# Optimization experiments

Measured on AMD Instinct MI355X. Metric: run time of the kernel, lower is better.

Reference implementation:

```python
import jax, jax.numpy as jnp
import numpy as np

TEMP = 0.07
NUM_CLASSES = 4

def setup_inputs() -> dict:
    key = jax.random.key(0)
    k1, k2 = jax.random.split(key)
    features_in = jax.random.normal(k1, (4, 64, 2048), dtype=jnp.float32)
    labels_in = jax.random.randint(k2, (4, 2048), 0, NUM_CLASSES, dtype=jnp.int64)
    return {"features_in": features_in, "labels_in": labels_in}

def reference(features_in, labels_in):
    B, C, N = features_in.shape
    M = B * N
    # torch .view(C, B*N): row-major reinterpret of contiguous [B,C,N]
    feats = features_in.reshape(C, M).T            # [M, C]
    labels = labels_in.reshape(-1)                 # [M]

    # per-class keep probability: min(750/(count+1), 1), gathered by label
    counts = jnp.bincount(labels, length=NUM_CLASSES)
    keep_p = jnp.minimum(750.0 / (counts.astype(jnp.float32) + 1.0), 1.0)
    p = keep_p[labels]                             # [M]
    sel = jax.random.bernoulli(jax.random.key(42), p)  # [M] bool, stochastic subsample

    # L2 normalize rows; original divides by norms of already-normalized rows (==1)
    nv = feats / jnp.linalg.norm(feats, axis=1, keepdims=True)
    sim = nv @ nv.T                                # [M, M] cosine similarities
    dp = jnp.exp(sim / TEMP)
    dp = dp * (1.0 - jnp.eye(M, dtype=dp.dtype))   # zero the diagonal

    same = labels[:, None] == labels[None, :]
    pair = sel[:, None] & sel[None, :]             # both points kept
    pos = jnp.sum(jnp.where(same & pair, dp, 0.0), axis=1)
    neg = jnp.sum(jnp.where((~same) & pair, dp, 0.0), axis=1)

    frac = pos / (pos + neg)
    per = -jnp.log(jnp.where(sel, frac, 1.0))      # guard unselected rows
    n_sel = jnp.maximum(jnp.sum(sel), 1)
    loss = jnp.sum(jnp.where(sel, per, 0.0)) / n_sel
    return loss
```

## Files before the change

### kernel.cpp

```cpp
#include <hip/hip_runtime.h>
#include <hip/hip_bf16.h>

#define M_TOT 8192
#define NCLS 4
#define NSEL_CAP 4096
#define NT 64

typedef __attribute__((ext_vector_type(8)))  short short8v;
typedef __attribute__((ext_vector_type(16))) float f32x16;

__device__ __forceinline__ void async_copy16(const void* gsrc, void* ldst) {
#if defined(__HIP_DEVICE_COMPILE__)
    __builtin_amdgcn_global_load_lds(
        (const __attribute__((address_space(1))) void*)gsrc,
        (__attribute__((address_space(3))) void*)ldst, 16, 0, 0);
#endif
}

__device__ __forceinline__ unsigned int rotl32(unsigned int x, unsigned int r) {
    return (x << r) | (x >> (32u - r));
}

__device__ __forceinline__ uint2 threefry_pair_key42(unsigned int j) {
    const unsigned int ks0 = 0u;
    const unsigned int ks1 = 42u;
    const unsigned int ks2 = 0x1BD11BDAu ^ 0u ^ 42u;
    unsigned int x0 = j + ks0;
    unsigned int x1 = (j + 4096u) + ks1;
#define TF_RND(r) { x0 += x1; x1 = rotl32(x1, (r)); x1 ^= x0; }
    TF_RND(13u) TF_RND(15u) TF_RND(26u) TF_RND(6u)
    x0 += ks1; x1 += ks2 + 1u;
    TF_RND(17u) TF_RND(29u) TF_RND(16u) TF_RND(24u)
    x0 += ks2; x1 += ks0 + 2u;
    TF_RND(13u) TF_RND(15u) TF_RND(26u) TF_RND(6u)
    x0 += ks0; x1 += ks1 + 3u;
    TF_RND(17u) TF_RND(29u) TF_RND(16u) TF_RND(24u)
    x0 += ks1; x1 += ks2 + 4u;
    TF_RND(13u) TF_RND(15u) TF_RND(26u) TF_RND(6u)
    x0 += ks2; x1 += ks0 + 5u;
#undef TF_RND
    return make_uint2(x0, x1);
}

__device__ __forceinline__ float bits_to_unit(unsigned int bits) {
    return __uint_as_float((bits >> 9) | 0x3F800000u) - 1.0f;
}

__device__ __forceinline__ unsigned short f2bf(float x) {
    const unsigned int u = __float_as_uint(x);
    return (unsigned short)((u + 0x7FFFu + ((u >> 16) & 1u)) >> 16);
}
__device__ __forceinline__ float bf2f(unsigned short b) {
    return __uint_as_float(((unsigned int)b) << 16);
}

#define NV_OFS(plane, c, p) (((((plane) << 3) + (c)) << 12) + (p))

__global__ __launch_bounds__(256) void select_norm_kernel(
        const float* __restrict__ features,
        const int* __restrict__ labels,
        int* __restrict__ nsel_g,
        int* __restrict__ lab_sel,
        unsigned short* __restrict__ nv,
        float* __restrict__ pos,
        float* __restrict__ neg) {
    __shared__ int   hist[NCLS];
    __shared__ float keepp[NCLS];
    __shared__ int   wtot[4];
    __shared__ int   lds_m[NSEL_CAP];
    const int t = threadIdx.x, b = blockIdx.x;
    const int lane = t & 63, w = t >> 6;

    const int gid = b * 256 + t;
    if (gid < NSEL_CAP) { pos[gid] = 0.0f; neg[gid] = 0.0f; }
    if (t < NCLS) hist[t] = 0;
    __syncthreads();

    {
        const int m0 = t * 32;
        int c0 = 0, c1 = 0, c2 = 0, c3 = 0;
        for (int r = 0; r < 32; ++r) {
            const int lab = labels[m0 + r];
            c0 += (lab == 0); c1 += (lab == 1); c2 += (lab == 2); c3 += (lab == 3);
        }
        int cc[4] = {c0, c1, c2, c3};
        #pragma unroll
        for (int cls = 0; cls < NCLS; ++cls) {
            int v = cc[cls];
            for (int off = 32; off > 0; off >>= 1) v += __shfl_down(v, off, 64);
            if (lane == 0) atomicAdd(&hist[cls], v);
        }
    }
    __syncthreads();
    if (t < NCLS) keepp[t] = fminf(750.0f / ((float)hist[t] + 1.0f), 1.0f);
    __syncthreads();

    const int jb = t * 16;
    unsigned int flags = 0u;
    int cnt = 0;
    for (int r = 0; r < 16; ++r) {
        const uint2 bb = threefry_pair_key42((unsigned int)(jb + r));
        if (bits_to_unit(bb.x) < keepp[labels[jb + r]])        { flags |= 1u << r;        ++cnt; }
        if (bits_to_unit(bb.y) < keepp[labels[jb + r + 4096]]) { flags |= 1u << (16 + r); ++cnt; }
    }
    int x = cnt;
    #pragma unroll
    for (int off = 1; off < 64; off <<= 1) {
        const int y = __shfl_up(x, off, 64);
        if (lane >= off) x += y;
    }
    if (lane == 63) wtot[w] = x;
    const int excl = x - cnt;
    __syncthreads();
    int base = excl;
    for (int w2 = 0; w2 < w; ++w2) base += wtot[w2];
    const int nsel = wtot[0] + wtot[1] + wtot[2] + wtot[3];
    if (b == 0 && t == 0) *nsel_g = nsel;
    for (int r = 0; r < 16; ++r) {
        if (flags & (1u << r))        lds_m[base++] = jb + r;
        if (flags & (1u << (16 + r))) lds_m[base++] = jb + r + 4096;
    }
    __syncthreads();

    const int p  = b * 32 + (t >> 3);
    const int kg = t & 7;
    if (p >= nsel) return;
    const int m = lds_m[p];
    if (kg == 0) lab_sel[p] = labels[m];
    float v[8];
    float ss = 0.0f;
    #pragma unroll
    for (int q = 0; q < 8; ++q) {
        v[q] = features[(kg * 8 + q) * M_TOT + m];
        ss += v[q] * v[q];
    }
    ss += __shfl_xor(ss, 1, 8);
    ss += __shfl_xor(ss, 2, 8);
    ss += __shfl_xor(ss, 4, 8);
    const float rn = rsqrtf(ss);
    unsigned short hs[8], ls[8];
    #pragma unroll
    for (int q = 0; q < 8; ++q) {
        const float xx = v[q] * rn;
        const unsigned short h = f2bf(xx);
        hs[q] = h;
        ls[q] = f2bf(xx - bf2f(h));
    }
    *(uint4*)&nv[NV_OFS(0, kg, p) * 8] = *(const uint4*)hs;
    *(uint4*)&nv[NV_OFS(1, kg, p) * 8] = *(const uint4*)ls;
}

#define EXP2_SCALE 20.609929155556605f

__global__ __launch_bounds__(256, 4) void pair_kernel(
        const unsigned short* __restrict__ nv,
        const int* __restrict__ lab_sel,
        const int* __restrict__ nsel_g,
        float* __restrict__ pos,
        float* __restrict__ neg) {
    const int nsel = *nsel_g;
    const int it = blockIdx.y, jt = blockIdx.x;
    const int i0 = it * 64, j0 = jt * 64;
    if (i0 >= nsel || j0 >= nsel) return;

    __shared__ __align__(16) unsigned short frags[2][2][8][64][8];
    __shared__ int La[64], Lb[64];

    const int t = threadIdx.x;
    const int wave = t >> 6, lane = t & 63;

    #pragma unroll
    for (int it8 = 0; it8 < 8; ++it8) {
        const int combo = it8 * 4 + wave;
        const int side  = combo >> 4;
        const int plane = (combo >> 3) & 1;
        const int c     = combo & 7;
        const int base0 = (side ? j0 : i0);
        async_copy16(&nv[NV_OFS(plane, c, base0 + lane) * 8],
                     &frags[side][plane][c][lane][0]);
    }
    if (t < 64)       La[t]      = lab_sel[i0 + t];
    else if (t < 128) Lb[t - 64] = lab_sel[j0 + t - 64];
    __syncthreads();

    const int qi = (wave >> 1) * 32, qj = (wave & 1) * 32;
    const int half = lane >> 5, l31 = lane & 31;
    const int ra = qi + l31, rb = qj + l31;

    f32x16 acc;
    #pragma unroll
    for (int r = 0; r < 16; ++r) acc[r] = 0.0f;

    #pragma unroll
    for (int s = 0; s < 4; ++s) {
        const int c = 2 * s + half;
        const short8v ah = *(const short8v*)&frags[0][0][c][ra][0];
        const short8v al = *(const short8v*)&frags[0][1][c][ra][0];
        const short8v bh = *(const short8v*)&frags[1][0][c][rb][0];
        const short8v bl = *(const short8v*)&frags[1][1][c][rb][0];
        acc = __builtin_amdgcn_mfma_f32_32x32x16_bf16(ah, bh, acc, 0, 0, 0);
        acc = __builtin_amdgcn_mfma_f32_32x32x16_bf16(ah, bl, acc, 0, 0, 0);
        acc = __builtin_amdgcn_mfma_f32_32x32x16_bf16(al, bh, acc, 0, 0, 0);
    }

    const int colL = qj + l31;
    const int jg = j0 + colL;
    const int Lj = Lb[colL];
    float cp = 0.0f, cn = 0.0f;
    #pragma unroll
    for (int r = 0; r < 16; ++r) {
        const int rowL = qi + (r & 3) + 8 * (r >> 2) + 4 * half;
        const int ig = i0 + rowL;
        const bool valid = (ig < nsel) && (jg < nsel) && (ig != jg);
        const float d = valid ? exp2f(acc[r] * EXP2_SCALE) : 0.0f;
        if (La[rowL] == Lj) cp += d; else cn += d;
    }
    cp += __shfl_xor(cp, 32, 64);
    cn += __shfl_xor(cn, 32, 64);
    if (half == 0 && jg < nsel) {
        atomicAdd(&pos[jg], cp);
        atomicAdd(&neg[jg], cn);
    }
}

__global__ void loss_kernel(const float* __restrict__ pos,
                            const float* __restrict__ neg,
                            const int* __restrict__ nsel_g,
                            float* __restrict__ out) {
    const int nsel = *nsel_g;
    float s = 0.0f;
    for (int i = threadIdx.x; i < nsel; i += 256) {
        const float fr = pos[i] / (pos[i] + neg[i]);
        s += -logf(fr);
    }
    __shared__ float red[256];
    red[threadIdx.x] = s;
    __syncthreads();
    for (int off = 128; off > 0; off >>= 1) {
        if (threadIdx.x < off) red[threadIdx.x] += red[threadIdx.x + off];
        __syncthreads();
    }
    if (threadIdx.x == 0) out[0] = red[0] / (float)(nsel > 0 ? nsel : 1);
}

extern "C" void kernel_launch(void* const* d_in, const int* in_sizes, int n_in,
                              void* d_out, int out_size, void* d_ws, size_t ws_size,
                              hipStream_t stream) {
    const float* features = (const float*)d_in[0];
    const int*   labels   = (const int*)d_in[1];
    float*       out      = (float*)d_out;
    char*        ws       = (char*)d_ws;

    int*   nsel_g   = (int*)(ws);
    int*   lab_sel  = (int*)(ws + 1024);
    float* pos      = (float*)(ws + 1024 + 16384);
    float* neg      = pos + NSEL_CAP;
    unsigned short* nv = (unsigned short*)(ws + 1024 + 16384 + 32768);

    select_norm_kernel<<<128, 256, 0, stream>>>(features, labels, nsel_g, lab_sel,
                                                nv, pos, neg);
    pair_kernel<<<dim3(NT, NT), 256, 0, stream>>>(nv, lab_sel, nsel_g, pos, neg);
    loss_kernel<<<1, 256, 0, stream>>>(pos, neg, nsel_g, out);
}
```

Before: 82.71 us.

## Normalize features by source tile with coalesced loads instead of gathered selections

```diff
diff --git a/kernel.cpp b/kernel.cpp
--- a/kernel.cpp
+++ b/kernel.cpp
@@ -67,13 +67,15 @@
     __shared__ int   hist[NCLS];
     __shared__ float keepp[NCLS];
     __shared__ int   wtot[4];
-    __shared__ int   lds_m[NSEL_CAP];
+    __shared__ int   slot_local[64];
+    __shared__ float tile[64][65];
     const int t = threadIdx.x, b = blockIdx.x;
     const int lane = t & 63, w = t >> 6;
 
     const int gid = b * 256 + t;
     if (gid < NSEL_CAP) { pos[gid] = 0.0f; neg[gid] = 0.0f; }
     if (t < NCLS) hist[t] = 0;
+    if (t < 64) slot_local[t] = -1;
     __syncthreads();
 
     {
@@ -117,37 +119,61 @@
     const int nsel = wtot[0] + wtot[1] + wtot[2] + wtot[3];
     if (b == 0 && t == 0) *nsel_g = nsel;
     for (int r = 0; r < 16; ++r) {
-        if (flags & (1u << r))        lds_m[base++] = jb + r;
-        if (flags & (1u << (16 + r))) lds_m[base++] = jb + r + 4096;
-    }
-    __syncthreads();
-
-    const int p  = b * 32 + (t >> 3);
+        if (flags & (1u << r)) {
+            const int m = jb + r;
+            lab_sel[base] = labels[m];
+            if ((m >> 6) == b) slot_local[m & 63] = base;
+            ++base;
+        }
+        if (flags & (1u << (16 + r))) {
+            const int m = jb + r + 4096;
+            lab_sel[base] = labels[m];
+            if ((m >> 6) == b) slot_local[m & 63] = base;
+            ++base;
+        }
+    }
+
+    #pragma unroll
+    for (int it4 = 0; it4 < 4; ++it4) {
+        const int idx = it4 * 256 + t;
+        const int c   = idx >> 4;
+        const int mg4 = (idx & 15) * 4;
+        const float4 v = *(const float4*)&features[c * M_TOT + b * 64 + mg4];
+        tile[c][mg4]     = v.x;
+        tile[c][mg4 + 1] = v.y;
+        tile[c][mg4 + 2] = v.z;
+        tile[c][mg4 + 3] = v.w;
+    }
+    __syncthreads();
+
     const int kg = t & 7;
-    if (p >= nsel) return;
-    const int m = lds_m[p];
-    if (kg == 0) lab_sel[p] = labels[m];
-    float v[8];
-    float ss = 0.0f;
-    #pragma unroll
-    for (int q = 0; q < 8; ++q) {
-        v[q] = features[(kg * 8 + q) * M_TOT + m];
-        ss += v[q] * v[q];
-    }
-    ss += __shfl_xor(ss, 1, 8);
-    ss += __shfl_xor(ss, 2, 8);
-    ss += __shfl_xor(ss, 4, 8);
-    const float rn = rsqrtf(ss);
-    unsigned short hs[8], ls[8];
-    #pragma unroll
-    for (int q = 0; q < 8; ++q) {
-        const float xx = v[q] * rn;
-        const unsigned short h = f2bf(xx);
-        hs[q] = h;
-        ls[q] = f2bf(xx - bf2f(h));
-    }
-    *(uint4*)&nv[NV_OFS(0, kg, p) * 8] = *(const uint4*)hs;
-    *(uint4*)&nv[NV_OFS(1, kg, p) * 8] = *(const uint4*)ls;
+    #pragma unroll
+    for (int pass = 0; pass < 2; ++pass) {
+        const int mm = pass * 32 + (t >> 3);
+        const int slot = slot_local[mm];
+        float v[8];
+        float ss = 0.0f;
+        #pragma unroll
+        for (int q = 0; q < 8; ++q) {
+            v[q] = tile[kg * 8 + q][mm];
+            ss += v[q] * v[q];
+        }
+        ss += __shfl_xor(ss, 1, 8);
+        ss += __shfl_xor(ss, 2, 8);
+        ss += __shfl_xor(ss, 4, 8);
+        if (slot < 0) continue;
+        const float rn = rsqrtf(ss);
+        unsigned short hs[8], ls[8];
+        #pragma unroll
+        for (int q = 0; q < 8; ++q) {
+            const float xx = v[q] * rn;
+            const unsigned short h = f2bf(xx);
+            hs[q] = h;
+            ls[q] = f2bf(xx - bf2f(h));
+        }
+        *(uint4*)&nv[NV_OFS(0, kg, slot) * 8] = *(const uint4*)hs;
+        *(uint4*)&nv[NV_OFS(1, kg, slot) * 8] = *(const uint4*)ls;
+    }
 }
 
 #define EXP2_SCALE 20.609929155556605f
```

After: 86.55 us. +4.6%, slower.
